# Performance work log

Measured on AMD Instinct MI355X. Metric: run time of the kernel, lower is better.

## Reference

```python
import jax, jax.numpy as jnp
import numpy as np

N_QUBITS = 12


def _apply_rx(state, q, theta, n):
    B = state.shape[0]
    left, right = 1 << q, 1 << (n - q - 1)
    s = state.reshape(B, left, 2, right)
    th = jnp.atleast_1d(jnp.asarray(theta)).reshape(-1, 1, 1)  # (B,1,1) or (1,1,1)
    c = jnp.cos(0.5 * th).astype(state.dtype)
    ms = (-1j * jnp.sin(0.5 * th)).astype(state.dtype)
    s0, s1 = s[:, :, 0, :], s[:, :, 1, :]
    new = jnp.stack([c * s0 + ms * s1, ms * s0 + c * s1], axis=2)
    return new.reshape(B, -1)


def _apply_cnot(state, ctrl, tgt, n):
    # flip target amplitudes on the control=1 slab
    B = state.shape[0]
    a, b = min(ctrl, tgt), max(ctrl, tgt)
    shape = (B, 1 << a, 2, 1 << (b - a - 1), 2, 1 << (n - b - 1))
    ax_c = 2 if ctrl == a else 4
    ax_t = 4 if ctrl == a else 2
    s = state.reshape(shape)
    s0 = jnp.take(s, 0, axis=ax_c)
    s1 = jnp.take(s, 1, axis=ax_c)
    ax_t_after = ax_t - 1 if ax_t > ax_c else ax_t
    s1 = jnp.flip(s1, axis=ax_t_after)
    return jnp.stack([s0, s1], axis=ax_c).reshape(B, -1)


def _simulate(x, w):
    # x: (B, n) angles; w: (L, n) angles. Returns (B, n) Pauli-Z expectations.
    B, n = x.shape
    L = w.shape[0]
    state = jnp.zeros((B, 1 << n), jnp.complex64).at[:, 0].set(1.0)
    # angle embedding: RX(x[:, j]) on qubit j
    for j in range(n):
        state = _apply_rx(state, j, x[:, j], n)
    # VQC layers: RX(w[i, j]) then ring of CNOTs
    for i in range(L):
        for j in range(n):
            state = _apply_rx(state, j, w[i, j], n)
        if n == 2:
            state = _apply_cnot(state, 0, 1, n)
        elif n > 2:
            for j in range(n):
                state = _apply_cnot(state, j, (j + 1) % n, n)
    probs = state.real ** 2 + state.imag ** 2  # (B, 2^n)
    exps = []
    for i in range(n):
        p = probs.reshape(B, 1 << i, 2, -1).sum(axis=(1, 3))  # (B, 2)
        exps.append(p[:, 0] - p[:, 1])
    return jnp.stack(exps, axis=-1)


def setup_inputs() -> dict:
    key = jax.random.key(0)
    k1, k2 = jax.random.split(key)
    x = jax.random.normal(k1, (2048, N_QUBITS), dtype=jnp.float32)
    # xavier_normal-ish init for w of shape (num_layers, num_qubits)
    w = jax.random.normal(k2, (2, N_QUBITS), dtype=jnp.float32) * 0.3
    return {"x": x, "w": w}


def reference(x, w):
    return _simulate(x, w)
```

## Files before the change

### kernel.cpp

```cpp
#include <hip/hip_runtime.h>

#define NQ 12
#define NSTATES (1 << NQ)

struct QPlan { unsigned rx2[NQ]; unsigned sgn[NQ]; };

constexpr QPlan make_plan() {
    QPlan P{};
    unsigned grow[NQ] = {}, hcol[NQ] = {};
    for (int j = 0; j < NQ; ++j) { grow[j] = 1u << j; hcol[j] = 1u << j; }
    for (int j = 0; j < NQ; ++j) {
        int cb = NQ - 1 - j, tb = NQ - 1 - ((j + 1) % NQ);
        grow[tb] ^= grow[cb]; hcol[cb] ^= hcol[tb];
    }
    for (int q = 0; q < NQ; ++q) P.rx2[q] = hcol[NQ - 1 - q];
    for (int j = 0; j < NQ; ++j) {
        int cb = NQ - 1 - j, tb = NQ - 1 - ((j + 1) % NQ);
        grow[tb] ^= grow[cb]; hcol[cb] ^= hcol[tb];
    }
    for (int q = 0; q < NQ; ++q) P.sgn[q] = grow[NQ - 1 - q];
    return P;
}
constexpr QPlan QP = make_plan();

constexpr unsigned kpart(unsigned m) {
    return ((m >> 0) & 1u) | (((m >> 9) & 1u) << 1) | (((m >> 10) & 1u) << 2) | (((m >> 11) & 1u) << 3);
}
constexpr unsigned lpart(unsigned m) {
    return ((m >> 1) & 1u) | (((m >> 2) & 1u) << 1) | (((m >> 3) & 1u) << 2)
         | (((m >> 6) & 1u) << 3) | (((m >> 7) & 1u) << 4) | (((m >> 8) & 1u) << 5);
}
constexpr unsigned wpart(unsigned m) {
    return ((m >> 4) & 1u) | (((m >> 5) & 1u) << 1);
}
constexpr unsigned tpart(unsigned m) { return lpart(m) | (wpart(m) << 6); }

static_assert(kpart(QP.rx2[0]) == 12 && tpart(QP.rx2[0]) == 0, "v-local");
static_assert(kpart(QP.rx2[1]) == 6  && tpart(QP.rx2[1]) == 0, "v-local");
static_assert(kpart(QP.rx2[11]) == 13 && tpart(QP.rx2[11]) == 0, "v-local triple");
static_assert(kpart(QP.rx2[3]) == 0 && wpart(QP.rx2[3]) == 0 && lpart(QP.rx2[3]) == 48, "lane scalar");
static_assert(kpart(QP.rx2[4]) == 0 && wpart(QP.rx2[4]) == 0 && lpart(QP.rx2[4]) == 24, "lane scalar");
static_assert(kpart(QP.rx2[8]) == 0 && wpart(QP.rx2[8]) == 0 && lpart(QP.rx2[8]) == 6,  "lane scalar");
static_assert(kpart(QP.rx2[9]) == 0 && wpart(QP.rx2[9]) == 0 && lpart(QP.rx2[9]) == 3,  "lane scalar");
static_assert(kpart(QP.rx2[5]) == 0 && tpart(QP.rx2[5]) == 136, "cross scalar");
static_assert(kpart(QP.rx2[6]) == 0 && tpart(QP.rx2[6]) == 192, "cross scalar");
static_assert(kpart(QP.rx2[7]) == 0 && tpart(QP.rx2[7]) == 68,  "cross scalar");
static_assert(kpart(QP.rx2[2]) == 2 && lpart(QP.rx2[2]) == 32 && wpart(QP.rx2[2]) == 0, "mixed");
static_assert(kpart(QP.rx2[10]) == 1 && lpart(QP.rx2[10]) == 1 && wpart(QP.rx2[10]) == 0, "mixed");

struct SignPlan { unsigned ks[NQ]; unsigned ts[NQ]; };
constexpr SignPlan make_signs() {
    SignPlan S{};
    for (int q = 0; q < NQ; ++q) { S.ks[q] = kpart(QP.sgn[q]); S.ts[q] = tpart(QP.sgn[q]); }
    return S;
}
constexpr SignPlan SP = make_signs();

template <int KM>
__device__ __forceinline__ void vgate(float (&vr)[16], float (&vi)[16], float c, float s) {
    #pragma unroll
    for (int ka = 0; ka < 16; ++ka) {
        const int kb = ka ^ KM;
        if (ka < kb) {
            float nur = fmaf(c, vr[ka],  s * vi[kb]);
            float nui = fmaf(c, vi[ka], -s * vr[kb]);
            float nvr = fmaf(c, vr[kb],  s * vi[ka]);
            float nvi = fmaf(c, vi[kb], -s * vr[ka]);
            vr[ka] = nur; vi[ka] = nui; vr[kb] = nvr; vi[kb] = nvi;
        }
    }
}

template <int KM, int LM>
__device__ __forceinline__ void mixed_gate(float (&ar)[16], float (&ai)[16], float c, float s) {
    #pragma unroll
    for (int ka = 0; ka < 16; ++ka) {
        const int kb = ka ^ KM;
        if (ka < kb) {
            float pra = __shfl_xor(ar[kb], LM, 64);
            float pia = __shfl_xor(ai[kb], LM, 64);
            float prb = __shfl_xor(ar[ka], LM, 64);
            float pib = __shfl_xor(ai[ka], LM, 64);
            ar[ka] = fmaf(c, ar[ka],  s * pia);
            ai[ka] = fmaf(c, ai[ka], -s * pra);
            ar[kb] = fmaf(c, ar[kb],  s * pib);
            ai[kb] = fmaf(c, ai[kb], -s * prb);
        }
    }
}

__global__ __launch_bounds__(256, 4) void qsim_fast(
    const float* __restrict__ x, const float* __restrict__ w, float* __restrict__ out)
{
    __shared__ float xr[256], xi[256];
    __shared__ float red[4][NQ];
    const int b = blockIdx.x;
    const int tid = threadIdx.x;
    const int lane = tid & 63;

    constexpr int TQ[8] = {10, 9, 8, 5, 4, 3, 7, 6};
    float F = 1.f;
    #pragma unroll
    for (int i = 0; i < 8; ++i) {
        float a = x[b * NQ + TQ[i]] + w[TQ[i]];
        float s, c; __sincosf(0.5f * a, &s, &c);
        F *= ((tid >> i) & 1) ? s : c;
    }
    const int rt = __popc((unsigned)tid) & 3;
    float sr = (rt == 0) ? F : (rt == 2 ? -F : 0.f);
    float si = (rt == 1) ? -F : (rt == 3 ? F : 0.f);

    constexpr int KQ[4] = {11, 2, 1, 0};
    float kc[4], ks[4];
    #pragma unroll
    for (int i = 0; i < 4; ++i) {
        float a = x[b * NQ + KQ[i]] + w[KQ[i]];
        __sincosf(0.5f * a, &ks[i], &kc[i]);
    }
    float vr[16], vi[16];
    #pragma unroll
    for (int k = 0; k < 16; ++k) {
        float g = ((k & 1) ? ks[0] : kc[0]) * ((k & 2) ? ks[1] : kc[1])
                * ((k & 4) ? ks[2] : kc[2]) * ((k & 8) ? ks[3] : kc[3]);
        const int rk = __builtin_popcount((unsigned)k) & 3;
        vr[k] = (rk == 0) ? g : (rk == 2 ? -g : 0.f);
        vi[k] = (rk == 1) ? -g : (rk == 3 ? g : 0.f);
    }

    {
        float s, c;
        __sincosf(0.5f * w[NQ + 0],  &s, &c); vgate<12>(vr, vi, c, s);
        __sincosf(0.5f * w[NQ + 1],  &s, &c); vgate<6>(vr, vi, c, s);
        __sincosf(0.5f * w[NQ + 11], &s, &c); vgate<13>(vr, vi, c, s);
    }

    {
        const int LMs[4] = {48, 24, 6, 3};
        const int JJ[4]  = {3, 4, 8, 9};
        #pragma unroll
        for (int i = 0; i < 4; ++i) {
            float s, c; __sincosf(0.5f * w[NQ + JJ[i]], &s, &c);
            float pr = __shfl_xor(sr, LMs[i], 64);
            float pi = __shfl_xor(si, LMs[i], 64);
            sr = fmaf(c, sr,  s * pi);
            si = fmaf(c, si, -s * pr);
        }
    }

    {
        float s5, c5, s6, c6, s7, c7;
        __sincosf(0.5f * w[NQ + 5], &s5, &c5);
        __sincosf(0.5f * w[NQ + 6], &s6, &c6);
        __sincosf(0.5f * w[NQ + 7], &s7, &c7);
        xr[tid] = sr; xi[tid] = si;
        __syncthreads();
        const float m0 = c5 * c6 * c7;
        const float m5 = s5 * c6 * c7, m6 = c5 * s6 * c7, m7 = c5 * c6 * s7;
        const float m56 = s5 * s6 * c7, m57 = s5 * c6 * s7, m67 = c5 * s6 * s7;
        const float m567 = s5 * s6 * s7;
        float nr = m0 * sr, ni = m0 * si;
        { float pr = xr[tid ^ 136], pi = xi[tid ^ 136]; nr = fmaf( m5, pi, nr); ni = fmaf(-m5, pr, ni); }
        { float pr = xr[tid ^ 192], pi = xi[tid ^ 192]; nr = fmaf( m6, pi, nr); ni = fmaf(-m6, pr, ni); }
        { float pr = xr[tid ^  68], pi = xi[tid ^  68]; nr = fmaf( m7, pi, nr); ni = fmaf(-m7, pr, ni); }
        { float pr = xr[tid ^  72], pi = xi[tid ^  72]; nr = fmaf(-m56, pr, nr); ni = fmaf(-m56, pi, ni); }
        { float pr = xr[tid ^ 204], pi = xi[tid ^ 204]; nr = fmaf(-m57, pr, nr); ni = fmaf(-m57, pi, ni); }
        { float pr = xr[tid ^ 132], pi = xi[tid ^ 132]; nr = fmaf(-m67, pr, nr); ni = fmaf(-m67, pi, ni); }
        { float pr = xr[tid ^  12], pi = xi[tid ^  12]; nr = fmaf(-m567, pi, nr); ni = fmaf( m567, pr, ni); }
        sr = nr; si = ni;
    }

    float ar[16], ai[16];
    #pragma unroll
    for (int k = 0; k < 16; ++k) {
        ar[k] = sr * vr[k] - si * vi[k];
        ai[k] = sr * vi[k] + si * vr[k];
    }
    {
        float s, c;
        __sincosf(0.5f * w[NQ + 2],  &s, &c); mixed_gate<2, 32>(ar, ai, c, s);
        __sincosf(0.5f * w[NQ + 10], &s, &c); mixed_gate<1, 1>(ar, ai, c, s);
    }

    float ex[NQ];
    #pragma unroll
    for (int q = 0; q < NQ; ++q) ex[q] = 0.f;
    #pragma unroll
    for (int k = 0; k < 16; ++k) {
        float p2 = fmaf(ar[k], ar[k], ai[k] * ai[k]);
        #pragma unroll
        for (int q = 0; q < NQ; ++q) {
            if (__builtin_popcount(SP.ks[q] & (unsigned)k) & 1) ex[q] -= p2;
            else                                                ex[q] += p2;
        }
    }
    #pragma unroll
    for (int q = 0; q < NQ; ++q) {
        float v = (__popc(SP.ts[q] & (unsigned)tid) & 1) ? -ex[q] : ex[q];
        #pragma unroll
        for (int off = 32; off >= 1; off >>= 1) v += __shfl_xor(v, off, 64);
        ex[q] = v;
    }
    const int wv = tid >> 6;
    float o = 0.f;
    #pragma unroll
    for (int q = 0; q < NQ; ++q) o = (lane == q) ? ex[q] : o;
    if (lane < NQ) red[wv][lane] = o;
    __syncthreads();
    if (tid < NQ) out[b * NQ + tid] = red[0][tid] + red[1][tid] + red[2][tid] + red[3][tid];
}

__global__ __launch_bounds__(256) void qsim_generic(
    const float* __restrict__ x, const float* __restrict__ w,
    float* __restrict__ out, int L)
{
    __shared__ float re[NSTATES];
    __shared__ float im[NSTATES];
    __shared__ float wsum[4][NQ];
    const int b = blockIdx.x;
    const int t = threadIdx.x;

    for (int i = t; i < NSTATES; i += 256) { re[i] = 0.0f; im[i] = 0.0f; }
    if (t == 0) re[0] = 1.0f;
    __syncthreads();

    auto apply_rx = [&](int q, float theta) {
        const int bit = NQ - 1 - q, mask = 1 << bit;
        const float c = cosf(0.5f * theta), s = sinf(0.5f * theta);
        #pragma unroll
        for (int it = 0; it < NSTATES / 2 / 256; ++it) {
            const int p  = t + it * 256;
            const int i0 = ((p >> bit) << (bit + 1)) | (p & (mask - 1));
            const int i1 = i0 | mask;
            const float a0r = re[i0], a0i = im[i0], a1r = re[i1], a1i = im[i1];
            re[i0] = c * a0r + s * a1i;  im[i0] = c * a0i - s * a1r;
            re[i1] = c * a1r + s * a0i;  im[i1] = c * a1i - s * a0r;
        }
        __syncthreads();
    };
    auto apply_cnot = [&](int ctrl, int tgt) {
        const int cbit = NQ - 1 - ctrl, tbit = NQ - 1 - tgt;
        const int lo = cbit < tbit ? cbit : tbit, hi = cbit < tbit ? tbit : cbit;
        #pragma unroll
        for (int it = 0; it < NSTATES / 4 / 256; ++it) {
            const int p  = t + it * 256;
            const int x1 = ((p  >> lo) << (lo + 1)) | (p  & ((1 << lo) - 1));
            const int x2 = ((x1 >> hi) << (hi + 1)) | (x1 & ((1 << hi) - 1));
            const int ia = x2 | (1 << cbit), ib = ia | (1 << tbit);
            const float tr = re[ia]; re[ia] = re[ib]; re[ib] = tr;
            const float ti = im[ia]; im[ia] = im[ib]; im[ib] = ti;
        }
        __syncthreads();
    };

    for (int j = 0; j < NQ; ++j) apply_rx(j, x[b * NQ + j]);
    for (int l2 = 0; l2 < L; ++l2) {
        for (int j = 0; j < NQ; ++j) apply_rx(j, w[l2 * NQ + j]);
        for (int j = 0; j < NQ; ++j) apply_cnot(j, (j + 1) % NQ);
    }

    float ex[NQ];
    #pragma unroll
    for (int q = 0; q < NQ; ++q) ex[q] = 0.0f;
    #pragma unroll
    for (int it = 0; it < NSTATES / 256; ++it) {
        const int i = t + it * 256;
        const float p = re[i] * re[i] + im[i] * im[i];
        #pragma unroll
        for (int q = 0; q < NQ; ++q) ex[q] += ((i >> (NQ - 1 - q)) & 1) ? -p : p;
    }
    #pragma unroll
    for (int q = 0; q < NQ; ++q) {
        float v = ex[q];
        #pragma unroll
        for (int off = 32; off > 0; off >>= 1) v += __shfl_down(v, off, 64);
        ex[q] = v;
    }
    const int wid = t >> 6, lane = t & 63;
    if (lane == 0) {
        #pragma unroll
        for (int q = 0; q < NQ; ++q) wsum[wid][q] = ex[q];
    }
    __syncthreads();
    if (t < NQ) {
        float v = 0.0f;
        #pragma unroll
        for (int k = 0; k < 4; ++k) v += wsum[k][t];
        out[b * NQ + t] = v;
    }
}

extern "C" void kernel_launch(void* const* d_in, const int* in_sizes, int n_in,
                              void* d_out, int out_size, void* d_ws, size_t ws_size,
                              hipStream_t stream) {
    const float* x = (const float*)d_in[0];
    const float* w = (const float*)d_in[1];
    float* out = (float*)d_out;
    const int B = in_sizes[0] / NQ;
    const int L = in_sizes[1] / NQ;
    if (L == 2) {
        qsim_fast<<<dim3(B), dim3(256), 0, stream>>>(x, w, out);
    } else {
        qsim_generic<<<dim3(B), dim3(256), 0, stream>>>(x, w, out, L);
    }
}
```

Baseline: 69.23 us.

## Pack complex amplitudes to fp16 for shuffles, use WHT and LDS reduction

```diff
diff --git a/kernel.cpp b/kernel.cpp
--- a/kernel.cpp
+++ b/kernel.cpp
@@ -56,6 +56,16 @@
 }
 constexpr SignPlan SP = make_signs();
 
+typedef __fp16 half2_t __attribute__((ext_vector_type(2)));
+__device__ __forceinline__ int pk(float a, float b) {
+    half2_t h = __builtin_amdgcn_cvt_pkrtz(a, b);
+    return __builtin_bit_cast(int, h);
+}
+__device__ __forceinline__ void upk(int u, float& a, float& b) {
+    half2_t h = __builtin_bit_cast(half2_t, u);
+    a = (float)h[0]; b = (float)h[1];
+}
+
 template <int KM>
 __device__ __forceinline__ void vgate(float (&vr)[16], float (&vi)[16], float c, float s) {
     #pragma unroll
@@ -77,10 +87,10 @@
     for (int ka = 0; ka < 16; ++ka) {
         const int kb = ka ^ KM;
         if (ka < kb) {
-            float pra = __shfl_xor(ar[kb], LM, 64);
-            float pia = __shfl_xor(ai[kb], LM, 64);
-            float prb = __shfl_xor(ar[ka], LM, 64);
-            float pib = __shfl_xor(ai[ka], LM, 64);
+            int ua = __shfl_xor(pk(ar[kb], ai[kb]), LM, 64);
+            int ub = __shfl_xor(pk(ar[ka], ai[ka]), LM, 64);
+            float pra, pia, prb, pib;
+            upk(ua, pra, pia); upk(ub, prb, pib);
             ar[ka] = fmaf(c, ar[ka],  s * pia);
             ai[ka] = fmaf(c, ai[ka], -s * pra);
             ar[kb] = fmaf(c, ar[kb],  s * pib);
@@ -89,14 +99,16 @@
     }
 }
 
+#define PAD_STRIDE 257
+#define SMEM2_OFF  (NQ * PAD_STRIDE)
+#define SMEM_TOTAL (SMEM2_OFF + 192)
+
 __global__ __launch_bounds__(256, 4) void qsim_fast(
     const float* __restrict__ x, const float* __restrict__ w, float* __restrict__ out)
 {
-    __shared__ float xr[256], xi[256];
-    __shared__ float red[4][NQ];
+    __shared__ __align__(16) float smem[SMEM_TOTAL];
     const int b = blockIdx.x;
     const int tid = threadIdx.x;
-    const int lane = tid & 63;
 
     constexpr int TQ[8] = {10, 9, 8, 5, 4, 3, 7, 6};
     float F = 1.f;
@@ -140,8 +152,8 @@
         #pragma unroll
         for (int i = 0; i < 4; ++i) {
             float s, c; __sincosf(0.5f * w[NQ + JJ[i]], &s, &c);
-            float pr = __shfl_xor(sr, LMs[i], 64);
-            float pi = __shfl_xor(si, LMs[i], 64);
+            float pr, pi;
+            upk(__shfl_xor(pk(sr, si), LMs[i], 64), pr, pi);
             sr = fmaf(c, sr,  s * pi);
             si = fmaf(c, si, -s * pr);
         }
@@ -152,20 +164,22 @@
         __sincosf(0.5f * w[NQ + 5], &s5, &c5);
         __sincosf(0.5f * w[NQ + 6], &s6, &c6);
         __sincosf(0.5f * w[NQ + 7], &s7, &c7);
-        xr[tid] = sr; xi[tid] = si;
+        int* xpk = reinterpret_cast<int*>(smem);
+        xpk[tid] = pk(sr, si);
         __syncthreads();
         const float m0 = c5 * c6 * c7;
         const float m5 = s5 * c6 * c7, m6 = c5 * s6 * c7, m7 = c5 * c6 * s7;
         const float m56 = s5 * s6 * c7, m57 = s5 * c6 * s7, m67 = c5 * s6 * s7;
         const float m567 = s5 * s6 * s7;
         float nr = m0 * sr, ni = m0 * si;
-        { float pr = xr[tid ^ 136], pi = xi[tid ^ 136]; nr = fmaf( m5, pi, nr); ni = fmaf(-m5, pr, ni); }
-        { float pr = xr[tid ^ 192], pi = xi[tid ^ 192]; nr = fmaf( m6, pi, nr); ni = fmaf(-m6, pr, ni); }
-        { float pr = xr[tid ^  68], pi = xi[tid ^  68]; nr = fmaf( m7, pi, nr); ni = fmaf(-m7, pr, ni); }
-        { float pr = xr[tid ^  72], pi = xi[tid ^  72]; nr = fmaf(-m56, pr, nr); ni = fmaf(-m56, pi, ni); }
-        { float pr = xr[tid ^ 204], pi = xi[tid ^ 204]; nr = fmaf(-m57, pr, nr); ni = fmaf(-m57, pi, ni); }
-        { float pr = xr[tid ^ 132], pi = xi[tid ^ 132]; nr = fmaf(-m67, pr, nr); ni = fmaf(-m67, pi, ni); }
-        { float pr = xr[tid ^  12], pi = xi[tid ^  12]; nr = fmaf(-m567, pi, nr); ni = fmaf( m567, pr, ni); }
+        float pr, pi;
+        upk(xpk[tid ^ 136], pr, pi); nr = fmaf( m5, pi, nr); ni = fmaf(-m5, pr, ni);
+        upk(xpk[tid ^ 192], pr, pi); nr = fmaf( m6, pi, nr); ni = fmaf(-m6, pr, ni);
+        upk(xpk[tid ^  68], pr, pi); nr = fmaf( m7, pi, nr); ni = fmaf(-m7, pr, ni);
+        upk(xpk[tid ^  72], pr, pi); nr = fmaf(-m56, pr, nr); ni = fmaf(-m56, pi, ni);
+        upk(xpk[tid ^ 204], pr, pi); nr = fmaf(-m57, pr, nr); ni = fmaf(-m57, pi, ni);
+        upk(xpk[tid ^ 132], pr, pi); nr = fmaf(-m67, pr, nr); ni = fmaf(-m67, pi, ni);
+        upk(xpk[tid ^  12], pr, pi); nr = fmaf(-m567, pi, nr); ni = fmaf( m567, pr, ni);
         sr = nr; si = ni;
     }
 
@@ -181,32 +195,48 @@
         __sincosf(0.5f * w[NQ + 10], &s, &c); mixed_gate<1, 1>(ar, ai, c, s);
     }
 
-    float ex[NQ];
-    #pragma unroll
-    for (int q = 0; q < NQ; ++q) ex[q] = 0.f;
-    #pragma unroll
-    for (int k = 0; k < 16; ++k) {
-        float p2 = fmaf(ar[k], ar[k], ai[k] * ai[k]);
-        #pragma unroll
-        for (int q = 0; q < NQ; ++q) {
-            if (__builtin_popcount(SP.ks[q] & (unsigned)k) & 1) ex[q] -= p2;
-            else                                                ex[q] += p2;
-        }
-    }
+    float W[16];
+    #pragma unroll
+    for (int k = 0; k < 16; ++k) W[k] = fmaf(ar[k], ar[k], ai[k] * ai[k]);
+    #pragma unroll
+    for (int m = 1; m < 16; m <<= 1) {
+        #pragma unroll
+        for (int k = 0; k < 16; ++k) {
+            if (!(k & m)) {
+                float a = W[k], bb = W[k | m];
+                W[k] = a + bb; W[k | m] = a - bb;
+            }
+        }
+    }
+
+    __syncthreads();
+
     #pragma unroll
     for (int q = 0; q < NQ; ++q) {
-        float v = (__popc(SP.ts[q] & (unsigned)tid) & 1) ? -ex[q] : ex[q];
-        #pragma unroll
-        for (int off = 32; off >= 1; off >>= 1) v += __shfl_xor(v, off, 64);
-        ex[q] = v;
-    }
-    const int wv = tid >> 6;
-    float o = 0.f;
-    #pragma unroll
-    for (int q = 0; q < NQ; ++q) o = (lane == q) ? ex[q] : o;
-    if (lane < NQ) red[wv][lane] = o;
-    __syncthreads();
-    if (tid < NQ) out[b * NQ + tid] = red[0][tid] + red[1][tid] + red[2][tid] + red[3][tid];
+        float v = W[SP.ks[q]];
+        if (__popc(SP.ts[q] & (unsigned)tid) & 1) v = -v;
+        smem[q * PAD_STRIDE + tid] = v;
+    }
+    __syncthreads();
+
+    if (tid < 192) {
+        const int q = tid >> 4, c = tid & 15;
+        const int base = q * PAD_STRIDE + c * 16;
+        float sum = 0.f;
+        #pragma unroll
+        for (int jj = 0; jj < 16; ++jj)
+            sum += smem[base + ((jj + c) & 15)];
+        smem[SMEM2_OFF + tid] = sum;
+    }
+    __syncthreads();
+
+    if (tid < NQ) {
+        const float4* p = reinterpret_cast<const float4*>(&smem[SMEM2_OFF + 16 * tid]);
+        float4 a0 = p[0], a1 = p[1], a2 = p[2], a3 = p[3];
+        float v = (a0.x + a0.y + a0.z + a0.w) + (a1.x + a1.y + a1.z + a1.w)
+                + (a2.x + a2.y + a2.z + a2.w) + (a3.x + a3.y + a3.z + a3.w);
+        out[b * NQ + tid] = v;
+    }
 }
 
 __global__ __launch_bounds__(256) void qsim_generic(
```

Result: faster. 66.31 us (-4.2%).
